# Kernel tuning notes

Measured on AMD Instinct MI355X. Metric: run time of the kernel, lower is better.

## Reference

```python
import jax, jax.numpy as jnp
import numpy as np
import math
from itertools import combinations

SEQ_LEN = 8
D_MODEL = 2048
OUT_DIM = 1152
WAY = 5
SHOT = 5
N_SUPPORT = WAY * SHOT
N_QUERIES = 200
TUPLES = np.array(list(combinations(range(SEQ_LEN), 2)), dtype=np.int32)  # [28, 2]
L = TUPLES.shape[0]  # 28 temporal tuples
PE_SCALE = 0.1
LN_EPS = 1e-5
COS_EPS = 1e-8


def _pos_encoding(seq, d):
    pos = jnp.arange(seq, dtype=jnp.float32)[:, None]
    div = jnp.exp(jnp.arange(0, d, 2, dtype=jnp.float32) * (-math.log(10000.0) / d))
    pe = jnp.zeros((seq, d), dtype=jnp.float32)
    pe = pe.at[:, 0::2].set(jnp.sin(pos * div) * PE_SCALE)
    pe = pe.at[:, 1::2].set(jnp.cos(pos * div) * PE_SCALE)
    return pe  # [seq, d]


def _layernorm(x, g, b):
    mu = x.mean(-1, keepdims=True)
    var = ((x - mu) ** 2).mean(-1, keepdims=True)
    return (x - mu) * jax.lax.rsqrt(var + LN_EPS) * g + b


def setup_inputs() -> dict:
    key = jax.random.key(0)
    ks = jax.random.split(key, 6)
    support_set = jax.random.normal(ks[0], (N_SUPPORT, SEQ_LEN, D_MODEL), jnp.float32)
    queries = jax.random.normal(ks[1], (N_QUERIES, SEQ_LEN, D_MODEL), jnp.float32)
    # sorted equal-shot episode: labels = [0]*5 + [1]*5 + ... + [4]*5
    support_labels = jnp.repeat(jnp.arange(WAY, dtype=jnp.int32), SHOT)
    k_w = jax.random.normal(ks[2], (OUT_DIM, 2 * D_MODEL), jnp.float32) * 0.02
    v_w = jax.random.normal(ks[3], (OUT_DIM, 2 * D_MODEL), jnp.float32) * 0.02
    k_b = jnp.zeros((OUT_DIM,), jnp.float32)
    v_b = jnp.zeros((OUT_DIM,), jnp.float32)
    ln_k_g = jnp.ones((OUT_DIM,), jnp.float32)
    ln_k_b = jnp.zeros((OUT_DIM,), jnp.float32)
    return {"support_set": support_set, "support_labels": support_labels,
            "queries": queries, "k_w": k_w, "k_b": k_b, "v_w": v_w, "v_b": v_b,
            "ln_k_g": ln_k_g, "ln_k_b": ln_k_b}


def reference(support_set, support_labels, queries, k_w, k_b, v_w, v_b, ln_k_g, ln_k_b):
    # dropout is inference-mode (identity)
    pe = _pos_encoding(SEQ_LEN, D_MODEL)
    sp = support_set + pe  # [Ns, S, D_MODEL]
    qp = queries + pe      # [Nq, S, D_MODEL]

    tup = jnp.asarray(TUPLES)
    # gather temporal tuples: [N, L, 2, D_MODEL] -> [N, L, 2*D_MODEL]
    s_t = sp[:, tup].reshape(N_SUPPORT, L, 2 * D_MODEL)
    q_t = qp[:, tup].reshape(N_QUERIES, L, 2 * D_MODEL)

    ks_s = _layernorm(s_t @ k_w.T + k_b, ln_k_g, ln_k_b)  # [Ns, L, OUT]
    ks_q = _layernorm(q_t @ k_w.T + k_b, ln_k_g, ln_k_b)  # [Nq, L, OUT]
    vs_s = s_t @ v_w.T + v_b                               # [Ns, L, OUT] (no norm, per original)
    vs_q = q_t @ v_w.T + v_b                               # [Nq, L, OUT]

    # labels are sorted equal-shot -> group by class via reshape
    ks_c = ks_s.reshape(WAY, SHOT, L, OUT_DIM)
    vs_c = vs_s.reshape(WAY, SHOT, L, OUT_DIM)

    # attention scores: [WAY, Nq, L(query tuple), SHOT, L(support tuple)]
    scores = jnp.einsum('qld,wsed->wqlse', ks_q, ks_c) / math.sqrt(OUT_DIM)
    attn = jax.nn.softmax(scores.reshape(WAY, N_QUERIES, L, SHOT * L), axis=-1)
    attn = attn.reshape(WAY, N_QUERIES, L, SHOT, L)
    # prototype: sum over shot of attn @ class_v -> [WAY, Nq, L, OUT]
    proto = jnp.einsum('wqlse,wsed->wqld', attn, vs_c)

    # query logits: -||q_v - proto||_F^2 / L per class
    diff = vs_q[None] - proto  # [WAY, Nq, L, OUT]
    ori = (-(diff ** 2).sum(axis=(-2, -1)) / L).T  # [Nq, WAY]

    # all_distances_tensor [Nq, L*OUT, WAY]
    A = jnp.transpose(proto, (1, 2, 3, 0)).reshape(N_QUERIES, L * OUT_DIM, WAY)
    num = jnp.einsum('qda,qdb->qab', A, A)            # [Nq, WAY, WAY]
    nrm = jnp.sqrt((A * A).sum(axis=1))               # [Nq, WAY]
    den = jnp.maximum(nrm[:, :, None] * nrm[:, None, :], COS_EPS)
    sim = num / den                                    # [Nq, WAY, WAY]
    return sim, ori
```

## Files before the change

### kernel.cpp

```cpp
#include <hip/hip_runtime.h>
#include <hip/hip_bf16.h>
#include <math.h>

typedef __hip_bfloat16 bf16;
typedef short s16x8 __attribute__((ext_vector_type(8)));
typedef float f32x4 __attribute__((ext_vector_type(4)));

#define NQ 200
#define SEQ 8
#define DM 2048
#define OUTD 1152
#define LT 28
#define M_ALL 6300
#define SM 5600
#define SN_PAD 768
#define ATT_STRIDE 720
#define N2 2304
#define KP 160
#define CH_Q 50
#define CH_ROWS 1400
#define CH_MPAD 1408
#define ABLK 144

__device__ __forceinline__ float bf2f(bf16 v) { return __bfloat162float(v); }
__device__ __forceinline__ bf16 f2bf(float v) { return __float2bfloat16(v); }
__device__ __forceinline__ float ubits2f(unsigned int u16) {
    unsigned int i = u16 << 16;
    float f; __builtin_memcpy(&f, &i, 4); return f;
}
__device__ __forceinline__ unsigned short f2bits(float f) {
    bf16 b = __float2bfloat16(f);
    unsigned short u; __builtin_memcpy(&u, &b, 2); return u;
}

__device__ const int TUP_A[LT] = {0,0,0,0,0,0,0,1,1,1,1,1,1,2,2,2,2,2,3,3,3,3,4,4,4,5,5,6};
__device__ const int TUP_B[LT] = {1,2,3,4,5,6,7,2,3,4,5,6,7,3,4,5,6,7,4,5,6,7,5,6,7,6,7,7};

__global__ __launch_bounds__(256) void wconv2_k(const float4* __restrict__ kw,
                                                const float4* __restrict__ vw,
                                                ushort4* __restrict__ o) {
    int i = blockIdx.x * 256 + threadIdx.x;
    float4 v = (i < 1179648) ? kw[i] : vw[i - 1179648];
    ushort4 r;
    r.x = f2bits(v.x); r.y = f2bits(v.y); r.z = f2bits(v.z); r.w = f2bits(v.w);
    o[i] = r;
}

__global__ __launch_bounds__(256) void pe_k(float* __restrict__ pe,
                                            bf16* __restrict__ attn_tail) {
    int i = blockIdx.x * 256 + threadIdx.x;
    int s = i >> 11, d = i & 2047;
    float dv = expf((float)(d & ~1) * (-9.210340371976184f / 2048.0f));
    float ang = (float)s * dv;
    pe[i] = (d & 1) ? cosf(ang) * 0.1f : sinf(ang) * 0.1f;
    for (int j = i; j < 32 * ATT_STRIDE; j += 64 * 256) attn_tail[j] = f2bf(0.f);
}

__global__ __launch_bounds__(256) void pex_k(const float* __restrict__ sup,
                                             const float* __restrict__ qry,
                                             const float* __restrict__ pe,
                                             bf16* __restrict__ pexb) {
    int r = blockIdx.x, t = threadIdx.x;
    int n, s;
    const float* src;
    if (r < 200) { n = r >> 3; s = r & 7; src = sup; }
    else { int rr = r - 200; n = rr >> 3; s = rr & 7; src = qry; }
    const float4* row = (const float4*)(src + ((size_t)n * SEQ + s) * DM);
    const float4* per = (const float4*)(pe + (size_t)s * DM);
    ushort4* orow = (ushort4*)(pexb + (size_t)r * DM);
    for (int d = t; d < DM / 4; d += 256) {
        float4 a = row[d], p = per[d];
        ushort4 o;
        o.x = f2bits(a.x + p.x); o.y = f2bits(a.y + p.y);
        o.z = f2bits(a.z + p.z); o.w = f2bits(a.w + p.w);
        orow[d] = o;
    }
}

template <int TN>
__global__ __launch_bounds__(256) void gemm_bt(
    const bf16* __restrict__ A, int lda, size_t aZ,
    const bf16* __restrict__ B, int ldb, size_t bZ,
    float scale, bf16* __restrict__ C, int ldc, size_t cZ, int K, int mlim) {
    constexpr int JN = TN / 32;
    const int gx = gridDim.x, gy = gridDim.y;
    const int nwg = gx * gy * (int)gridDim.z;
    const int orig = ((int)blockIdx.z * gy + blockIdx.y) * gx + blockIdx.x;
    const int qc = nwg >> 3, rc = nwg & 7;
    const int xcd = orig & 7, sub = orig >> 3;
    const int lg = (xcd < rc ? xcd * (qc + 1) : rc * (qc + 1) + (xcd - rc) * qc) + sub;
    const int bx = lg % gx;
    const int rest = lg / gx;
    const int by = rest % gy, bz = rest / gy;

    const unsigned short* Ag0 = (const unsigned short*)A + aZ * bz;
    const unsigned short* Bg0 = (const unsigned short*)B + bZ * bz;
    const size_t cbase = cZ * bz;
    const int tile_m = bx * 128, tile_n = by * TN;
    __shared__ unsigned short As[4 * 128 * 8];
    __shared__ unsigned short Bs[4 * TN * 8];
    const int t = threadIdx.x, lane = t & 63, wave = t >> 6;
    const int wm = (wave & 1) * 64, wn = (wave >> 1) * (TN / 2);
    const int srow = t >> 1, sq0 = (t & 1) * 2;
    const unsigned short* Ag = Ag0 + (size_t)(tile_m + srow) * lda + (t & 1) * 16;
    unsigned short* AsW0 = &As[((sq0 + 0) * 128 + srow) * 8];
    unsigned short* AsW1 = &As[((sq0 + 1) * 128 + srow) * 8];
    const unsigned short* Bg;
    unsigned short* BsW0;
    unsigned short* BsW1 = nullptr;
    if constexpr (TN == 128) {
        Bg = Bg0 + (size_t)(tile_n + srow) * ldb + (t & 1) * 16;
        BsW0 = &Bs[((sq0 + 0) * 128 + srow) * 8];
        BsW1 = &Bs[((sq0 + 1) * 128 + srow) * 8];
    } else {
        Bg = Bg0 + (size_t)(tile_n + (t >> 2)) * ldb + (t & 3) * 8;
        BsW0 = &Bs[((t & 3) * 64 + (t >> 2)) * 8];
    }
    const int fr = lane & 15, quad = lane >> 4;

    f32x4 acc[4][JN];
#pragma unroll
    for (int i = 0; i < 4; i++)
#pragma unroll
        for (int j = 0; j < JN; j++) acc[i][j] = {0.f, 0.f, 0.f, 0.f};

    for (int k0 = 0; k0 < K; k0 += 32) {
        uint4 a0 = *(const uint4*)(Ag + k0);
        uint4 a1 = *(const uint4*)(Ag + k0 + 8);
        uint4 b0 = *(const uint4*)(Bg + k0);
        uint4 b1;
        if constexpr (TN == 128) b1 = *(const uint4*)(Bg + k0 + 8);
        __syncthreads();
        *(uint4*)AsW0 = a0; *(uint4*)AsW1 = a1;
        *(uint4*)BsW0 = b0;
        if constexpr (TN == 128) *(uint4*)BsW1 = b1;
        __syncthreads();
        s16x8 af[4], bfv[JN];
#pragma unroll
        for (int i = 0; i < 4; i++)
            af[i] = *(const s16x8*)&As[(quad * 128 + wm + i * 16 + fr) * 8];
#pragma unroll
        for (int j = 0; j < JN; j++)
            bfv[j] = *(const s16x8*)&Bs[(quad * TN + wn + j * 16 + fr) * 8];
#pragma unroll
        for (int i = 0; i < 4; i++)
#pragma unroll
            for (int j = 0; j < JN; j++)
                acc[i][j] = __builtin_amdgcn_mfma_f32_16x16x32_bf16(af[i], bfv[j], acc[i][j], 0, 0, 0);
    }

    const int rb = quad * 4;
#pragma unroll
    for (int i = 0; i < 4; i++)
#pragma unroll
        for (int j = 0; j < JN; j++) {
            const int col = tile_n + wn + j * 16 + fr;
#pragma unroll
            for (int r = 0; r < 4; r++) {
                const int row = tile_m + wm + i * 16 + rb + r;
                if (row < mlim)
                    C[cbase + (size_t)row * ldc + col] = f2bf(acc[i][j][r] * scale);
            }
        }
}

__global__ __launch_bounds__(256) void combine_kv(
    const unsigned int* __restrict__ Yk, const unsigned int* __restrict__ Yv,
    const float* __restrict__ kb, const float* __restrict__ vb,
    const float* __restrict__ lng, const float* __restrict__ lnb,
    bf16* __restrict__ ks, bf16* __restrict__ vs) {
    const int t = threadIdx.x, lane = t & 63, wave = t >> 6;
    int orig = blockIdx.x;
    const bool vpath = orig >= M_ALL;
    if (vpath) orig -= M_ALL;
    {
        const int qc = M_ALL >> 3, rc = M_ALL & 7;
        const int xcd = orig & 7, sub = orig >> 3;
        orig = (xcd < rc ? xcd * (qc + 1) : rc * (qc + 1) + (xcd - rc) * qc) + sub;
    }
    const int m = orig;
    int mm = m < 700 ? m : m - 700;
    int base = m < 700 ? 0 : 200;
    int nsamp = mm / LT, l = mm - nsamp * LT;
    const unsigned int* Y = vpath ? Yv : Yk;
    const uint4* ya4 = (const uint4*)(Y + (size_t)(base + nsamp * 8 + TUP_A[l]) * (N2 / 2));
    const uint4* yb4 = (const uint4*)(Y + (size_t)(base + nsamp * 8 + TUP_B[l]) * (N2 / 2));
    if (vpath) {
        const float4* vb4 = (const float4*)vb;
        for (int u = t; u < OUTD / 4; u += 256) {
            uint4 a4 = ya4[u], b4 = yb4[u];
            float4 c4 = vb4[u];
            ushort4 o;
            o.x = f2bits(ubits2f(a4.x & 0xFFFFu) + ubits2f(b4.x >> 16) + c4.x);
            o.y = f2bits(ubits2f(a4.y & 0xFFFFu) + ubits2f(b4.y >> 16) + c4.y);
            o.z = f2bits(ubits2f(a4.z & 0xFFFFu) + ubits2f(b4.z >> 16) + c4.z);
            o.w = f2bits(ubits2f(a4.w & 0xFFFFu) + ubits2f(b4.w >> 16) + c4.w);
            *(ushort4*)&vs[(size_t)m * OUTD + u * 4] = o;
        }
        return;
    }
    const float4* kb4 = (const float4*)kb;
    float vals[8];
    int cnt = 0;
    float s = 0.f, s2 = 0.f;
    for (int u = t; u < OUTD / 4; u += 256) {
        uint4 a4 = ya4[u], b4 = yb4[u];
        float4 c4 = kb4[u];
        float v0 = ubits2f(a4.x & 0xFFFFu) + ubits2f(b4.x >> 16) + c4.x;
        float v1 = ubits2f(a4.y & 0xFFFFu) + ubits2f(b4.y >> 16) + c4.y;
        float v2 = ubits2f(a4.z & 0xFFFFu) + ubits2f(b4.z >> 16) + c4.z;
        float v3 = ubits2f(a4.w & 0xFFFFu) + ubits2f(b4.w >> 16) + c4.w;
        vals[cnt] = v0; vals[cnt + 1] = v1; vals[cnt + 2] = v2; vals[cnt + 3] = v3;
        cnt += 4;
        s += (v0 + v1) + (v2 + v3);
        s2 += v0 * v0 + v1 * v1 + v2 * v2 + v3 * v3;
    }
    for (int o = 32; o > 0; o >>= 1) { s += __shfl_xor(s, o); s2 += __shfl_xor(s2, o); }
    __shared__ float r1[4], r2[4];
    if (lane == 0) { r1[wave] = s; r2[wave] = s2; }
    __syncthreads();
    s = r1[0] + r1[1] + r1[2] + r1[3];
    s2 = r2[0] + r2[1] + r2[2] + r2[3];
    float mu = s * (1.f / OUTD);
    float var = s2 * (1.f / OUTD) - mu * mu;
    float inv = rsqrtf(fmaxf(var, 0.f) + 1e-5f);
    const float4* lg4 = (const float4*)lng;
    const float4* lb4 = (const float4*)lnb;
    cnt = 0;
    for (int u = t; u < OUTD / 4; u += 256) {
        float4 g4 = lg4[u], b4v = lb4[u];
        ushort4 o;
        o.x = f2bits((vals[cnt]     - mu) * inv * g4.x + b4v.x);
        o.y = f2bits((vals[cnt + 1] - mu) * inv * g4.y + b4v.y);
        o.z = f2bits((vals[cnt + 2] - mu) * inv * g4.z + b4v.z);
        o.w = f2bits((vals[cnt + 3] - mu) * inv * g4.w + b4v.w);
        cnt += 4;
        *(ushort4*)&ks[(size_t)m * OUTD + u * 4] = o;
    }
}

__global__ __launch_bounds__(320) void sv_k(const bf16* __restrict__ sc,
                                            bf16* __restrict__ attn,
                                            const bf16* __restrict__ vs,
                                            bf16* __restrict__ vp,
                                            float* __restrict__ gbuf) {
    const int t = threadIdx.x;
    if (blockIdx.x < SM) {
        const int row = blockIdx.x, w = t >> 6, lane = t & 63;
        const bf16* src = sc + (size_t)row * SN_PAD + w * 140;
        bf16* dst = attn + (size_t)row * ATT_STRIDE + w * ABLK;
        float a = bf2f(src[lane]);
        float b = bf2f(src[lane + 64]);
        float c = (lane < 12) ? bf2f(src[lane + 128]) : -3.0e38f;
        float m = fmaxf(fmaxf(a, b), c);
        for (int o = 32; o > 0; o >>= 1) m = fmaxf(m, __shfl_xor(m, o));
        float ea = __expf(a - m), eb = __expf(b - m);
        float ec = (lane < 12) ? __expf(c - m) : 0.f;
        float s = ea + eb + ec;
        for (int o = 32; o > 0; o >>= 1) s += __shfl_xor(s, o);
        float inv = 1.f / s;
        dst[lane] = f2bf(ea * inv);
        dst[lane + 64] = f2bf(eb * inv);
        if (lane < 16) dst[lane + 128] = f2bf(lane < 12 ? ec * inv : 0.f);
        return;
    }
    const int vb = blockIdx.x - SM;
    if (vb == 0)
        for (int i = t; i < NQ * 21; i += 320) gbuf[i] = 0.f;
    int idx = vb * 320 + t;
    int j = idx % KP;
    int rest = idx / KP;
    int dcol = rest % OUTD;
    int w = rest / OUTD;
    vp[idx] = (j < 140) ? vs[(size_t)(w * 140 + j) * OUTD + dcol] : f2bf(0.f);
}

__global__ __launch_bounds__(256) void gramred_k(const bf16* __restrict__ protoc,
                                                 const bf16* __restrict__ vs,
                                                 float* __restrict__ gbuf,
                                                 int row0, int q0) {
    const int ql = blockIdx.x;
    const int lgb = blockIdx.y;
    const int t = threadIdx.x, lane = t & 63, wave = t >> 6;
    const size_t PZ = (size_t)CH_MPAD * OUTD;
    float g[15] = {0.f};
    float h[5] = {0.f, 0.f, 0.f, 0.f, 0.f};
    float e = 0.f;
    for (int idx = t; idx < 2 * OUTD / 8; idx += 256) {
        int li = idx / 144;
        int dv = idx - li * 144;
        int l = lgb * 2 + li;
        size_t ml = (size_t)(ql * LT + l) * OUTD + dv * 8;
        s16x8 pw0 = *(const s16x8*)&protoc[0 * PZ + ml];
        s16x8 pw1 = *(const s16x8*)&protoc[1 * PZ + ml];
        s16x8 pw2 = *(const s16x8*)&protoc[2 * PZ + ml];
        s16x8 pw3 = *(const s16x8*)&protoc[3 * PZ + ml];
        s16x8 pw4 = *(const s16x8*)&protoc[4 * PZ + ml];
        s16x8 vv = *(const s16x8*)&vs[(size_t)(700 + row0 + ql * LT + l) * OUTD + dv * 8];
#pragma unroll
        for (int ee = 0; ee < 8; ee++) {
            float pv[5];
            pv[0] = ubits2f((unsigned short)pw0[ee]);
            pv[1] = ubits2f((unsigned short)pw1[ee]);
            pv[2] = ubits2f((unsigned short)pw2[ee]);
            pv[3] = ubits2f((unsigned short)pw3[ee]);
            pv[4] = ubits2f((unsigned short)pw4[ee]);
            float v = ubits2f((unsigned short)vv[ee]);
            e += v * v;
            int c = 0;
#pragma unroll
            for (int a = 0; a < 5; a++) {
                h[a] += v * pv[a];
#pragma unroll
                for (int b = a; b < 5; b++) g[c++] += pv[a] * pv[b];
            }
        }
    }
    float vals[21];
#pragma unroll
    for (int k = 0; k < 15; k++) vals[k] = g[k];
#pragma unroll
    for (int k = 0; k < 5; k++) vals[15 + k] = h[k];
    vals[20] = e;
#pragma unroll
    for (int k = 0; k < 21; k++)
        for (int o = 32; o > 0; o >>= 1) vals[k] += __shfl_xor(vals[k], o);
    __shared__ float red[4][21];
    if (lane == 0)
#pragma unroll
        for (int k = 0; k < 21; k++) red[wave][k] = vals[k];
    __syncthreads();
    if (t < 21) {
        float s = red[0][t] + red[1][t] + red[2][t] + red[3][t];
        atomicAdd(&gbuf[(q0 + ql) * 21 + t], s);
    }
}

__global__ __launch_bounds__(64) void out_k(const float* __restrict__ gbuf,
                                            float* __restrict__ out) {
    int q = blockIdx.x;
    if (threadIdx.x != 0) return;
    const float* r = gbuf + q * 21;
    float G[5][5];
    int c = 0;
    for (int a = 0; a < 5; a++)
        for (int b = a; b < 5; b++) { G[a][b] = r[c]; G[b][a] = r[c]; c++; }
    float e = r[20];
    float nrm[5];
    for (int a = 0; a < 5; a++) nrm[a] = sqrtf(fmaxf(G[a][a], 0.f));
    for (int a = 0; a < 5; a++)
        for (int b = 0; b < 5; b++)
            out[(size_t)q * 25 + a * 5 + b] = G[a][b] / fmaxf(nrm[a] * nrm[b], 1e-8f);
    for (int w = 0; w < 5; w++)
        out[5000 + (size_t)q * 5 + w] = -(e - 2.f * r[15 + w] + G[w][w]) * (1.f / 28.f);
}

extern "C" void kernel_launch(void* const* d_in, const int* in_sizes, int n_in,
                              void* d_out, int out_size, void* d_ws, size_t ws_size,
                              hipStream_t stream) {
    const float* sup = (const float*)d_in[0];
    const float* qry = (const float*)d_in[2];
    const float* k_w = (const float*)d_in[3];
    const float* k_b = (const float*)d_in[4];
    const float* v_w = (const float*)d_in[5];
    const float* v_b = (const float*)d_in[6];
    const float* lng = (const float*)d_in[7];
    const float* lnb = (const float*)d_in[8];
    (void)in_sizes; (void)n_in; (void)out_size; (void)ws_size;

    char* ws = (char*)d_ws;
    bf16* pexb   = (bf16*)(ws + 0);
    bf16* wbf    = (bf16*)(ws + 7864320);
    bf16* Yk     = (bf16*)(ws + 26738688);
    bf16* Yv     = (bf16*)(ws + 35033088);
    bf16* ks     = (bf16*)(ws + 0);
    bf16* vs     = (bf16*)(ws + 16220160);
    bf16* sc     = (bf16*)(ws + 30735360);
    bf16* vsp    = (bf16*)(ws + 39386112);
    bf16* attn   = (bf16*)(ws + 41229312);
    float* gbuf  = (float*)(ws + 49339392);
    float* pe    = (float*)(ws + 49356192);
    bf16* protoc = (bf16*)(ws + 0);

    pe_k<<<dim3(64), dim3(256), 0, stream>>>(pe, attn + (size_t)SM * ATT_STRIDE);
    pex_k<<<dim3(1800), dim3(256), 0, stream>>>(sup, qry, pe, pexb);
    wconv2_k<<<dim3(9216), dim3(256), 0, stream>>>(
        (const float4*)k_w, (const float4*)v_w, (ushort4*)wbf);

    gemm_bt<128><<<dim3(15, 18, 2), dim3(256), 0, stream>>>(
        pexb, DM, 0, wbf, DM, (size_t)4718592,
        1.0f, Yk, N2, (size_t)4147200, DM, 1800);

    combine_kv<<<dim3(2 * M_ALL), dim3(256), 0, stream>>>(
        (const unsigned int*)Yk, (const unsigned int*)Yv,
        k_b, v_b, lng, lnb, ks, vs);

    gemm_bt<64><<<dim3(44, 12, 1), dim3(256), 0, stream>>>(
        ks + (size_t)700 * OUTD, OUTD, 0, ks, OUTD, 0,
        0.029462782549439484f, sc, SN_PAD, 0, OUTD, 5632);

    sv_k<<<dim3(SM + 2880), dim3(320), 0, stream>>>(sc, attn, vs, vsp, gbuf);

    for (int c = 0; c < 4; c++) {
        gemm_bt<64><<<dim3(11, 18, 5), dim3(256), 0, stream>>>(
            attn + (size_t)c * CH_ROWS * ATT_STRIDE, ATT_STRIDE, (size_t)ABLK,
            vsp, KP, (size_t)OUTD * KP,
            1.0f, protoc, OUTD, (size_t)CH_MPAD * OUTD, KP, CH_MPAD);
        gramred_k<<<dim3(CH_Q, 14), dim3(256), 0, stream>>>(
            protoc, vs, gbuf, c * CH_ROWS, c * CH_Q);
    }

    out_k<<<dim3(NQ), dim3(64), 0, stream>>>(gbuf, (float*)d_out);
}
```

Measured before the change: 320.4 us.

## Fuse prototype GEMM with Gram reduction into one MFMA kernel

Replaces the four chunked passes of a prototype GEMM followed by a Gram/cross-term reduction with one fused kernel. Each block computes a 28x128 tile of all five class prototypes in registers with MFMA, then accumulates the 21 Gram, cross and norm terms directly. This removes the bf16 prototype round trip through global memory and seven extra launches. It also adds an XCD-aware block remap. The cost is a very small per-block GEMM (M=28 padded to 32) that reloads attention and value tiles for each of the 9 column tiles, and prototypes now stay in fp32 rather than being rounded to bf16.

After: 293.7 us. -8.3%, faster.

```diff
diff --git a/kernel.cpp b/kernel.cpp
--- a/kernel.cpp
+++ b/kernel.cpp
@@ -17,9 +17,6 @@
 #define ATT_STRIDE 720
 #define N2 2304
 #define KP 160
-#define CH_Q 50
-#define CH_ROWS 1400
-#define CH_MPAD 1408
 #define ABLK 144
 
 __device__ __forceinline__ float bf2f(bf16 v) { return __bfloat162float(v); }
@@ -275,65 +272,111 @@
     vp[idx] = (j < 140) ? vs[(size_t)(w * 140 + j) * OUTD + dcol] : f2bf(0.f);
 }
 
-__global__ __launch_bounds__(256) void gramred_k(const bf16* __restrict__ protoc,
-                                                 const bf16* __restrict__ vs,
-                                                 float* __restrict__ gbuf,
-                                                 int row0, int q0) {
-    const int ql = blockIdx.x;
-    const int lgb = blockIdx.y;
+__global__ __launch_bounds__(256) void fproto_k(
+    const bf16* __restrict__ attn,
+    const bf16* __restrict__ vsp,
+    const bf16* __restrict__ vs,
+    float* __restrict__ gbuf) {
+    const int nwg = gridDim.x;
+    int orig = blockIdx.x;
+    {
+        const int qc = nwg >> 3, rc = nwg & 7;
+        const int xcd = orig & 7, sub = orig >> 3;
+        orig = (xcd < rc ? xcd * (qc + 1) : rc * (qc + 1) + (xcd - rc) * qc) + sub;
+    }
+    const int q = orig / 9, dt = orig - q * 9;
     const int t = threadIdx.x, lane = t & 63, wave = t >> 6;
-    const size_t PZ = (size_t)CH_MPAD * OUTD;
-    float g[15] = {0.f};
-    float h[5] = {0.f, 0.f, 0.f, 0.f, 0.f};
-    float e = 0.f;
-    for (int idx = t; idx < 2 * OUTD / 8; idx += 256) {
-        int li = idx / 144;
-        int dv = idx - li * 144;
-        int l = lgb * 2 + li;
-        size_t ml = (size_t)(ql * LT + l) * OUTD + dv * 8;
-        s16x8 pw0 = *(const s16x8*)&protoc[0 * PZ + ml];
-        s16x8 pw1 = *(const s16x8*)&protoc[1 * PZ + ml];
-        s16x8 pw2 = *(const s16x8*)&protoc[2 * PZ + ml];
-        s16x8 pw3 = *(const s16x8*)&protoc[3 * PZ + ml];
-        s16x8 pw4 = *(const s16x8*)&protoc[4 * PZ + ml];
-        s16x8 vv = *(const s16x8*)&vs[(size_t)(700 + row0 + ql * LT + l) * OUTD + dv * 8];
-#pragma unroll
-        for (int ee = 0; ee < 8; ee++) {
-            float pv[5];
-            pv[0] = ubits2f((unsigned short)pw0[ee]);
-            pv[1] = ubits2f((unsigned short)pw1[ee]);
-            pv[2] = ubits2f((unsigned short)pw2[ee]);
-            pv[3] = ubits2f((unsigned short)pw3[ee]);
-            pv[4] = ubits2f((unsigned short)pw4[ee]);
-            float v = ubits2f((unsigned short)vv[ee]);
-            e += v * v;
-            int c = 0;
-#pragma unroll
-            for (int a = 0; a < 5; a++) {
-                h[a] += v * pv[a];
-#pragma unroll
-                for (int b = a; b < 5; b++) g[c++] += pv[a] * pv[b];
+    const int fr = lane & 15, quad = lane >> 4;
+
+    __shared__ unsigned short As[20 * 32 * 8];
+    __shared__ unsigned short Bs[20 * 128 * 8];
+    __shared__ float red[4][21];
+
+    const unsigned short* attn_u = (const unsigned short*)attn;
+    const unsigned short* vsp_u = (const unsigned short*)vsp;
+
+    f32x4 acc[5][2][2];
+#pragma unroll
+    for (int w = 0; w < 5; w++)
+#pragma unroll
+        for (int i = 0; i < 2; i++)
+#pragma unroll
+            for (int j = 0; j < 2; j++) acc[w][i][j] = {0.f, 0.f, 0.f, 0.f};
+
+#pragma unroll
+    for (int w = 0; w < 5; w++) {
+        __syncthreads();
+#pragma unroll
+        for (int i = 0; i < 3; i++) {
+            int slot = t + 256 * i;
+            if (slot < 640) {
+                int kq = slot >> 5, row = slot & 31;
+                *(uint4*)&As[slot * 8] =
+                    *(const uint4*)&attn_u[(size_t)(q * 28 + row) * ATT_STRIDE + w * ABLK + kq * 8];
             }
         }
-    }
-    float vals[21];
-#pragma unroll
-    for (int k = 0; k < 15; k++) vals[k] = g[k];
-#pragma unroll
-    for (int k = 0; k < 5; k++) vals[15 + k] = h[k];
-    vals[20] = e;
+#pragma unroll
+        for (int i = 0; i < 10; i++) {
+            int slot = t + 256 * i;
+            int kq = slot >> 7, drow = slot & 127;
+            *(uint4*)&Bs[slot * 8] =
+                *(const uint4*)&vsp_u[(size_t)(w * OUTD + dt * 128 + drow) * KP + kq * 8];
+        }
+        __syncthreads();
+#pragma unroll
+        for (int s = 0; s < 5; s++) {
+            s16x8 af[2], bfv[2];
+#pragma unroll
+            for (int i = 0; i < 2; i++)
+                af[i] = *(const s16x8*)&As[((s * 4 + quad) * 32 + i * 16 + fr) * 8];
+#pragma unroll
+            for (int j = 0; j < 2; j++)
+                bfv[j] = *(const s16x8*)&Bs[((s * 4 + quad) * 128 + wave * 32 + j * 16 + fr) * 8];
+#pragma unroll
+            for (int i = 0; i < 2; i++)
+#pragma unroll
+                for (int j = 0; j < 2; j++)
+                    acc[w][i][j] = __builtin_amdgcn_mfma_f32_16x16x32_bf16(af[i], bfv[j], acc[w][i][j], 0, 0, 0);
+        }
+    }
+
+    float st[21];
+#pragma unroll
+    for (int k = 0; k < 21; k++) st[k] = 0.f;
+#pragma unroll
+    for (int i = 0; i < 2; i++)
+#pragma unroll
+        for (int r = 0; r < 4; r++) {
+            const int l = i * 16 + quad * 4 + r;
+            if (l < 28) {
+                const size_t vrow = (size_t)(700 + q * 28 + l) * OUTD;
+#pragma unroll
+                for (int j = 0; j < 2; j++) {
+                    const int col = dt * 128 + wave * 32 + j * 16 + fr;
+                    float v = bf2f(vs[vrow + col]);
+                    float pv[5];
+#pragma unroll
+                    for (int w = 0; w < 5; w++) pv[w] = acc[w][i][j][r];
+                    st[20] += v * v;
+                    int c = 0;
+#pragma unroll
+                    for (int a = 0; a < 5; a++) {
+                        st[15 + a] += v * pv[a];
+#pragma unroll
+                        for (int b = a; b < 5; b++) st[c++] += pv[a] * pv[b];
+                    }
+                }
+            }
+        }
 #pragma unroll
     for (int k = 0; k < 21; k++)
-        for (int o = 32; o > 0; o >>= 1) vals[k] += __shfl_xor(vals[k], o);
-    __shared__ float red[4][21];
+        for (int o = 32; o > 0; o >>= 1) st[k] += __shfl_xor(st[k], o);
     if (lane == 0)
 #pragma unroll
-        for (int k = 0; k < 21; k++) red[wave][k] = vals[k];
+        for (int k = 0; k < 21; k++) red[wave][k] = st[k];
     __syncthreads();
-    if (t < 21) {
-        float s = red[0][t] + red[1][t] + red[2][t] + red[3][t];
-        atomicAdd(&gbuf[(q0 + ql) * 21 + t], s);
-    }
+    if (t < 21)
+        atomicAdd(&gbuf[q * 21 + t], red[0][t] + red[1][t] + red[2][t] + red[3][t]);
 }
 
 __global__ __launch_bounds__(64) void out_k(const float* __restrict__ gbuf,
@@ -380,7 +423,6 @@
     bf16* attn   = (bf16*)(ws + 41229312);
     float* gbuf  = (float*)(ws + 49339392);
     float* pe    = (float*)(ws + 49356192);
-    bf16* protoc = (bf16*)(ws + 0);
 
     pe_k<<<dim3(64), dim3(256), 0, stream>>>(pe, attn + (size_t)SM * ATT_STRIDE);
     pex_k<<<dim3(1800), dim3(256), 0, stream>>>(sup, qry, pe, pexb);
@@ -401,14 +443,7 @@
 
     sv_k<<<dim3(SM + 2880), dim3(320), 0, stream>>>(sc, attn, vs, vsp, gbuf);
 
-    for (int c = 0; c < 4; c++) {
-        gemm_bt<64><<<dim3(11, 18, 5), dim3(256), 0, stream>>>(
-            attn + (size_t)c * CH_ROWS * ATT_STRIDE, ATT_STRIDE, (size_t)ABLK,
-            vsp, KP, (size_t)OUTD * KP,
-            1.0f, protoc, OUTD, (size_t)CH_MPAD * OUTD, KP, CH_MPAD);
-        gramred_k<<<dim3(CH_Q, 14), dim3(256), 0, stream>>>(
-            protoc, vs, gbuf, c * CH_ROWS, c * CH_Q);
-    }
+    fproto_k<<<dim3(1800), dim3(256), 0, stream>>>(attn, vsp, vs, gbuf);
 
     out_k<<<dim3(NQ), dim3(64), 0, stream>>>(gbuf, (float*)d_out);
 }
```
